# Kernel tuning notes

Hardware: AMD Instinct MI355X
Metric: run time of the kernel (lower is better)

The kernel has to match this reference:

```python
import jax, jax.numpy as jnp
import numpy as np

B, S, D, H, DH = 8, 1024, 768, 12, 64
INIT_STD = 0.02
IGNORE = -100000.0


def setup_inputs() -> dict:
    key = jax.random.key(0)
    ks = jax.random.split(key, 5)
    return {
        "normalized_resid_pre": jax.random.normal(ks[0], (B, S, D), dtype=jnp.float32),
        "W_Q": jax.random.normal(ks[1], (H, D, DH), dtype=jnp.float32) * INIT_STD,
        "b_Q": jnp.zeros((H, DH), dtype=jnp.float32),
        "W_K": jax.random.normal(ks[2], (H, D, DH), dtype=jnp.float32) * INIT_STD,
        "b_K": jnp.zeros((H, DH), dtype=jnp.float32),
        "W_V": jax.random.normal(ks[3], (H, D, DH), dtype=jnp.float32) * INIT_STD,
        "b_V": jnp.zeros((H, DH), dtype=jnp.float32),
        "W_O": jax.random.normal(ks[4], (H, DH, D), dtype=jnp.float32) * INIT_STD,
        "b_O": jnp.zeros((D,), dtype=jnp.float32),
    }


def reference(normalized_resid_pre, W_Q, b_Q, W_K, b_K, W_V, b_V, W_O, b_O):
    x = normalized_resid_pre  # [B,S,D]
    q = jnp.einsum('bsd,hde->bshe', x, W_Q) + b_Q  # [B,S,H,DH]
    k = jnp.einsum('bsd,hde->bshe', x, W_K) + b_K
    v = jnp.einsum('bsd,hde->bshe', x, W_V) + b_V
    scores = jnp.einsum('bqhe,bkhe->bhqk', q, k) / jnp.sqrt(jnp.float32(DH))
    causal = jnp.triu(jnp.ones((S, S), dtype=bool), k=1)  # True above diagonal
    scores = jnp.where(causal, jnp.float32(IGNORE), scores)
    pattern = jax.nn.softmax(scores, axis=-1)  # [B,H,S,S]
    z = jnp.einsum('bhqk,bkhe->bqhe', pattern, v)  # [B,S,H,DH]
    attn_out = jnp.einsum('bqhe,hed->bqd', z, W_O) + b_O  # [B,S,D]
    return attn_out
```

## Files before the change

kernel.cpp:

```cpp
#include <hip/hip_runtime.h>
#include <hip/hip_bf16.h>
#include <stdint.h>

#define BB 8
#define SS 1024
#define DD 768
#define HH 12
#define DHH 64
#define BS (BB*SS)
#define NQKV (3*HH*DHH)

typedef __attribute__((ext_vector_type(8))) short bf16x8;
typedef __attribute__((ext_vector_type(4))) float f32x4;
typedef __attribute__((ext_vector_type(4))) unsigned int u32x4;

typedef const __attribute__((address_space(1))) unsigned int gu32;
typedef __attribute__((address_space(3))) unsigned int lu32;

static __device__ __forceinline__ unsigned short f2bf(float f) {
    union { float f; unsigned int u; } v; v.f = f;
    unsigned int u = v.u;
    unsigned int r = (u + 0x7fffu + ((u >> 16) & 1u)) >> 16;
    return (unsigned short)r;
}

static __device__ __forceinline__ unsigned int cvt_pk_bf16(float lo, float hi) {
    unsigned int r;
    asm("v_cvt_pk_bf16_f32 %0, %1, %2" : "=v"(r) : "v"(lo), "v"(hi));
    return r;
}


__global__ void k_f32_to_bf16(const float* __restrict__ in, unsigned short* __restrict__ out, int n) {
    int i = (blockIdx.x * 256 + threadIdx.x) * 4;
    if (i + 3 < n) {
        float4 v = *reinterpret_cast<const float4*>(in + i);
        ushort4 o;
        o.x = f2bf(v.x); o.y = f2bf(v.y); o.z = f2bf(v.z); o.w = f2bf(v.w);
        *reinterpret_cast<ushort4*>(out + i) = o;
    } else {
        for (; i < n; ++i) out[i] = f2bf(in[i]);
    }
}

__global__ void k_transpose_wqkv(const float* __restrict__ wq, const float* __restrict__ wk,
                                 const float* __restrict__ wv, unsigned short* __restrict__ wt) {
    __shared__ float tl[64][65];
    int rt = blockIdx.x;
    int z = blockIdx.y;
    int mat = z / 12, h = z - mat * 12;
    const float* src = ((mat == 0) ? wq : (mat == 1) ? wk : wv) + (size_t)h * 768 * 64;
    int d0 = rt * 64;
    int t = threadIdx.x;
    int row = t >> 4, c4 = (t & 15) * 4;
    #pragma unroll
    for (int p = 0; p < 4; ++p) {
        int d = p * 16 + row;
        float4 v = *reinterpret_cast<const float4*>(&src[(size_t)(d0 + d) * 64 + c4]);
        tl[d][c4 + 0] = v.x; tl[d][c4 + 1] = v.y; tl[d][c4 + 2] = v.z; tl[d][c4 + 3] = v.w;
    }
    __syncthreads();
    unsigned short* dstb = wt + ((size_t)(mat * 768 + h * 64)) * 768;
    #pragma unroll
    for (int p = 0; p < 4; ++p) {
        int e = p * 16 + row;
        ushort4 o;
        o.x = f2bf(tl[c4 + 0][e]); o.y = f2bf(tl[c4 + 1][e]);
        o.z = f2bf(tl[c4 + 2][e]); o.w = f2bf(tl[c4 + 3][e]);
        *reinterpret_cast<ushort4*>(&dstb[(size_t)e * 768 + d0 + c4]) = o;
    }
}

__global__ void k_transpose_wo(const float* __restrict__ wo, unsigned short* __restrict__ wot) {
    __shared__ float tl[64][65];
    int r0 = blockIdx.x * 64;
    int c0 = blockIdx.y * 64;
    int t = threadIdx.x;
    int row = t >> 4, c4 = (t & 15) * 4;
    #pragma unroll
    for (int p = 0; p < 4; ++p) {
        int r = p * 16 + row;
        float4 v = *reinterpret_cast<const float4*>(&wo[(size_t)(r0 + r) * 768 + c0 + c4]);
        tl[r][c4 + 0] = v.x; tl[r][c4 + 1] = v.y; tl[r][c4 + 2] = v.z; tl[r][c4 + 3] = v.w;
    }
    __syncthreads();
    #pragma unroll
    for (int p = 0; p < 4; ++p) {
        int c = p * 16 + row;
        ushort4 o;
        o.x = f2bf(tl[c4 + 0][c]); o.y = f2bf(tl[c4 + 1][c]);
        o.z = f2bf(tl[c4 + 2][c]); o.w = f2bf(tl[c4 + 3][c]);
        *reinterpret_cast<ushort4*>(&wot[(size_t)(c0 + c) * 768 + r0 + c4]) = o;
    }
}

__global__ void k_transpose_v(const unsigned short* __restrict__ vb, unsigned short* __restrict__ vtb) {
    __shared__ unsigned short tl[64][68];
    int s0 = blockIdx.x * 64;
    int bh = blockIdx.y;
    const unsigned short* src = vb + (size_t)bh * SS * DHH;
    unsigned short* dst = vtb + (size_t)bh * DHH * SS;
    int t = threadIdx.x;
    #pragma unroll
    for (int i = 0; i < 16; ++i) {
        int idx = t + i * 256;
        int sl = idx >> 6, e = idx & 63;
        tl[sl][e] = src[(size_t)(s0 + sl) * DHH + e];
    }
    __syncthreads();
    #pragma unroll
    for (int i = 0; i < 16; ++i) {
        int idx = t + i * 256;
        int e = idx >> 6, sl = idx & 63;
        dst[(size_t)e * SS + s0 + sl] = tl[sl][e];
    }
}


__launch_bounds__(256)
__global__ void k_gemm_qkv(const unsigned short* __restrict__ xb,
                           const unsigned short* __restrict__ wt,
                           const float* __restrict__ bq, const float* __restrict__ bk,
                           const float* __restrict__ bv,
                           unsigned short* __restrict__ qb,
                           unsigned short* __restrict__ kb,
                           unsigned short* __restrict__ vb) {
    __shared__ unsigned short As[2][128 * 32];
    __shared__ unsigned short Bs[2][128 * 32];
    int r0 = blockIdx.x * 128;
    int c0 = blockIdx.y * 128;
    int t = threadIdx.x;
    int w = t >> 6, l = t & 63;
    int lr = l & 15, lg = l >> 4;
    int wr = w >> 1, wc = w & 1;
    int srow = l >> 2;
    int g8 = (((l & 3) - (l >> 3)) & 3) * 8;

    auto STAGE = [&](int buf, int k0) {
        #pragma unroll
        for (int c = 0; c < 2; ++c) {
            int seg = w * 2 + c;
            int row = seg * 16 + srow;
            __builtin_amdgcn_global_load_lds(
                (gu32*)(xb + (size_t)(r0 + row) * DD + k0 + g8),
                (lu32*)&As[buf][seg * 512], 16, 0, 0);
            __builtin_amdgcn_global_load_lds(
                (gu32*)(wt + (size_t)(c0 + row) * DD + k0 + g8),
                (lu32*)&Bs[buf][seg * 512], 16, 0, 0);
        }
    };

    f32x4 acc[4][4] = {};
    STAGE(0, 0);
    __syncthreads();
    int rdo = ((lg + (lr >> 1)) & 3) * 8;
    for (int kk = 0; kk < 24; ++kk) {
        int cur = kk & 1;
        if (kk < 23) STAGE(cur ^ 1, kk * 32 + 32);
        bf16x8 af[4], bfr[4];
        #pragma unroll
        for (int m = 0; m < 4; ++m)
            af[m] = *reinterpret_cast<const bf16x8*>(&As[cur][(wr * 64 + m * 16 + lr) * 32 + rdo]);
        #pragma unroll
        for (int n = 0; n < 4; ++n)
            bfr[n] = *reinterpret_cast<const bf16x8*>(&Bs[cur][(wc * 64 + n * 16 + lr) * 32 + rdo]);
        #pragma unroll
        for (int m = 0; m < 4; ++m)
            #pragma unroll
            for (int n = 0; n < 4; ++n)
                acc[m][n] = __builtin_amdgcn_mfma_f32_16x16x32_bf16(af[m], bfr[n], acc[m][n], 0, 0, 0);
        __syncthreads();
    }
    #pragma unroll
    for (int n = 0; n < 4; ++n) {
        int c = c0 + wc * 64 + n * 16 + lr;
        int mat = c / 768;
        int within = c - mat * 768;
        int h = within >> 6, e = within & 63;
        const float* bptr = (mat == 0) ? bq : (mat == 1) ? bk : bv;
        float bias = bptr[within];
        unsigned short* dst = (mat == 0) ? qb : (mat == 1) ? kb : vb;
        #pragma unroll
        for (int m = 0; m < 4; ++m) {
            #pragma unroll
            for (int i = 0; i < 4; ++i) {
                int r = r0 + wr * 64 + m * 16 + lg * 4 + i;
                int b_ = r >> 10, s_ = r & 1023;
                dst[(((size_t)(b_ * HH + h)) * SS + s_) * DHH + e] = f2bf(acc[m][n][i] + bias);
            }
        }
    }
}


#define PW 34

__launch_bounds__(256, 3)
__global__ void k_attn(const unsigned short* __restrict__ qb,
                       const unsigned short* __restrict__ kb,
                       const unsigned short* __restrict__ vtb,
                       unsigned short* __restrict__ zb) {
    __shared__ unsigned short Ks[2][64 * 64];
    __shared__ unsigned short Vs[2][64 * 64];
    __shared__ unsigned int Pl[4][16 * PW];
    int id = blockIdx.x;
    int p = id / 96;
    int bh = id - p * 96;
    int qi = 15 - p;
    int q0 = qi * 64;

    int t = threadIdx.x, w = t >> 6, l = t & 63;
    int lr = l & 15, lg = l >> 4;
    const unsigned short* Qh = qb + (size_t)bh * SS * DHH;
    const unsigned short* Kh = kb + (size_t)bh * SS * DHH;
    const unsigned short* Vt = vtb + (size_t)bh * DHH * SS;
    int b_ = bh / HH, h = bh - b_ * HH;
    unsigned int* Pw = &Pl[w][0];

    int sr8 = l >> 3;
    int sc = ((l & 7) ^ sr8) * 8;

    auto STAGE = [&](int buf, int kbase) {
        #pragma unroll
        for (int c = 0; c < 2; ++c) {
            int seg = w * 2 + c;
            int row = seg * 8 + sr8;
            __builtin_amdgcn_global_load_lds(
                (gu32*)(Kh + (size_t)(kbase + row) * DHH + sc),
                (lu32*)&Ks[buf][seg * 512], 16, 0, 0);
            __builtin_amdgcn_global_load_lds(
                (gu32*)(Vt + (size_t)row * SS + kbase + sc),
                (lu32*)&Vs[buf][seg * 512], 16, 0, 0);
        }
    };

    int qabs = q0 + w * 16 + lr;
    STAGE(0, 0);
    bf16x8 qf[2];
    qf[0] = *reinterpret_cast<const bf16x8*>(Qh + (size_t)qabs * DHH + lg * 8);
    qf[1] = *reinterpret_cast<const bf16x8*>(Qh + (size_t)qabs * DHH + 32 + lg * 8);

    float m_r = -3.0e38f, l_r = 0.f;
    f32x4 zacc[4] = {};
    __syncthreads();

    for (int kt = 0; kt <= qi; ++kt) {
        int k0 = kt * 64;
        int cur = kt & 1;
        if (kt < qi) STAGE(cur ^ 1, k0 + 64);

        f32x4 sac[4] = {};
        #pragma unroll
        for (int ks = 0; ks < 2; ++ks) {
            #pragma unroll
            for (int ct = 0; ct < 4; ++ct) {
                bf16x8 kfr = *reinterpret_cast<const bf16x8*>(
                    &Ks[cur][(ct * 16 + lr) * 64 + (((ks * 4 + lg) ^ (lr & 7)) * 8)]);
                sac[ct] = __builtin_amdgcn_mfma_f32_16x16x32_bf16(kfr, qf[ks], sac[ct], 0, 0, 0);
            }
        }
        bool diag = (kt == qi);
        float sv[4][4];
        float pm = -3.0e38f;
        #pragma unroll
        for (int ct = 0; ct < 4; ++ct) {
            #pragma unroll
            for (int i = 0; i < 4; ++i) {
                float x = sac[ct][i] * 0.125f;
                if (diag) {
                    int kabs = k0 + ct * 16 + lg * 4 + i;
                    if (kabs > qabs) x = -3.0e38f;
                }
                sv[ct][i] = x;
                pm = fmaxf(pm, x);
            }
        }
        pm = fmaxf(pm, __shfl_xor(pm, 16));
        pm = fmaxf(pm, __shfl_xor(pm, 32));

        if (!__all(pm <= m_r + 8.f)) {
            float mn = fmaxf(m_r, pm);
            float alpha = __expf(m_r - mn);
            m_r = mn;
            l_r *= alpha;
            float aC[4];
            #pragma unroll
            for (int i = 0; i < 4; ++i) aC[i] = __shfl(alpha, lg * 4 + i);
            #pragma unroll
            for (int et = 0; et < 4; ++et)
                #pragma unroll
                for (int i = 0; i < 4; ++i) zacc[et][i] *= aC[i];
        }

        float ps = 0.f;
        #pragma unroll
        for (int ct = 0; ct < 4; ++ct) {
            float p0 = __expf(sv[ct][0] - m_r);
            float p1 = __expf(sv[ct][1] - m_r);
            float p2 = __expf(sv[ct][2] - m_r);
            float p3 = __expf(sv[ct][3] - m_r);
            ps += (p0 + p1) + (p2 + p3);
            unsigned int pk0 = cvt_pk_bf16(p0, p1);
            unsigned int pk1 = cvt_pk_bf16(p2, p3);
            *reinterpret_cast<uint2*>(&Pw[lr * PW + ct * 8 + lg * 2]) = make_uint2(pk0, pk1);
        }
        ps += __shfl_xor(ps, 16);
        ps += __shfl_xor(ps, 32);
        l_r += ps;

        #pragma unroll
        for (int ks = 0; ks < 2; ++ks) {
            bf16x8 pa = *reinterpret_cast<const bf16x8*>(&Pw[lr * PW + ks * 16 + lg * 4]);
            #pragma unroll
            for (int et = 0; et < 4; ++et) {
                bf16x8 vf = *reinterpret_cast<const bf16x8*>(
                    &Vs[cur][(et * 16 + lr) * 64 + (((ks * 4 + lg) ^ (lr & 7)) * 8)]);
                zacc[et] = __builtin_amdgcn_mfma_f32_16x16x32_bf16(pa, vf, zacc[et], 0, 0, 0);
            }
        }
        __syncthreads();
    }

    float lC[4];
    #pragma unroll
    for (int i = 0; i < 4; ++i) lC[i] = __shfl(l_r, lg * 4 + i);
    #pragma unroll
    for (int et = 0; et < 4; ++et) {
        #pragma unroll
        for (int i = 0; i < 4; ++i) {
            int r = q0 + w * 16 + lg * 4 + i;
            float z = zacc[et][i] / lC[i];
            zb[((size_t)(b_ * SS + r)) * DD + h * DHH + et * 16 + lr] = f2bf(z);
        }
    }
}


__launch_bounds__(256)
__global__ void k_gemm_out(const unsigned short* __restrict__ zb,
                           const unsigned short* __restrict__ wot,
                           const float* __restrict__ bo,
                           float* __restrict__ out) {
    __shared__ unsigned short As[2][128 * 32];
    __shared__ unsigned short Bs[2][128 * 32];
    int r0 = blockIdx.x * 128;
    int c0 = blockIdx.y * 128;
    int t = threadIdx.x;
    int w = t >> 6, l = t & 63;
    int lr = l & 15, lg = l >> 4;
    int wr = w >> 1, wc = w & 1;
    int srow = l >> 2;
    int g8 = (((l & 3) - (l >> 3)) & 3) * 8;

    auto STAGE = [&](int buf, int k0) {
        #pragma unroll
        for (int c = 0; c < 2; ++c) {
            int seg = w * 2 + c;
            int row = seg * 16 + srow;
            __builtin_amdgcn_global_load_lds(
                (gu32*)(zb + (size_t)(r0 + row) * DD + k0 + g8),
                (lu32*)&As[buf][seg * 512], 16, 0, 0);
            __builtin_amdgcn_global_load_lds(
                (gu32*)(wot + (size_t)(c0 + row) * DD + k0 + g8),
                (lu32*)&Bs[buf][seg * 512], 16, 0, 0);
        }
    };

    f32x4 acc[4][4] = {};
    STAGE(0, 0);
    __syncthreads();
    int rdo = ((lg + (lr >> 1)) & 3) * 8;
    for (int kk = 0; kk < 24; ++kk) {
        int cur = kk & 1;
        if (kk < 23) STAGE(cur ^ 1, kk * 32 + 32);
        bf16x8 af[4], bfr[4];
        #pragma unroll
        for (int m = 0; m < 4; ++m)
            af[m] = *reinterpret_cast<const bf16x8*>(&As[cur][(wr * 64 + m * 16 + lr) * 32 + rdo]);
        #pragma unroll
        for (int n = 0; n < 4; ++n)
            bfr[n] = *reinterpret_cast<const bf16x8*>(&Bs[cur][(wc * 64 + n * 16 + lr) * 32 + rdo]);
        #pragma unroll
        for (int m = 0; m < 4; ++m)
            #pragma unroll
            for (int n = 0; n < 4; ++n)
                acc[m][n] = __builtin_amdgcn_mfma_f32_16x16x32_bf16(af[m], bfr[n], acc[m][n], 0, 0, 0);
        __syncthreads();
    }
    #pragma unroll
    for (int n = 0; n < 4; ++n) {
        int c = c0 + wc * 64 + n * 16 + lr;
        float bias = bo[c];
        #pragma unroll
        for (int m = 0; m < 4; ++m) {
            #pragma unroll
            for (int i = 0; i < 4; ++i) {
                int r = r0 + wr * 64 + m * 16 + lg * 4 + i;
                out[(size_t)r * DD + c] = acc[m][n][i] + bias;
            }
        }
    }
}


extern "C" void kernel_launch(void* const* d_in, const int* in_sizes, int n_in,
                              void* d_out, int out_size, void* d_ws, size_t ws_size,
                              hipStream_t stream) {
    const float* x  = (const float*)d_in[0];
    const float* wq = (const float*)d_in[1];
    const float* bq = (const float*)d_in[2];
    const float* wk = (const float*)d_in[3];
    const float* bk = (const float*)d_in[4];
    const float* wv = (const float*)d_in[5];
    const float* bv = (const float*)d_in[6];
    const float* wo = (const float*)d_in[7];
    const float* bo = (const float*)d_in[8];
    float* out = (float*)d_out;

    char* ws = (char*)d_ws;
    size_t off = 0;
    auto alloc = [&](size_t bytes) -> char* {
        char* p = ws + off;
        off += (bytes + 255) & ~(size_t)255;
        return p;
    };
    unsigned short* xb   = (unsigned short*)alloc((size_t)BS * DD * 2);
    unsigned short* wt   = (unsigned short*)alloc((size_t)NQKV * DD * 2);
    unsigned short* wot  = (unsigned short*)alloc((size_t)DD * DD * 2);
    unsigned short* qb   = (unsigned short*)alloc((size_t)BB * HH * SS * DHH * 2);
    unsigned short* kb   = (unsigned short*)alloc((size_t)BB * HH * SS * DHH * 2);
    unsigned short* vb   = (unsigned short*)alloc((size_t)BB * HH * SS * DHH * 2);
    unsigned short* vtb  = (unsigned short*)alloc((size_t)BB * HH * SS * DHH * 2);
    unsigned short* zb   = (unsigned short*)alloc((size_t)BS * DD * 2);
    (void)ws_size; (void)in_sizes; (void)n_in; (void)out_size;

    k_f32_to_bf16<<<dim3((BS * DD) / (256 * 4)), dim3(256), 0, stream>>>(x, xb, BS * DD);
    k_transpose_wqkv<<<dim3(12, 36), dim3(256), 0, stream>>>(wq, wk, wv, wt);
    k_transpose_wo<<<dim3(12, 12), dim3(256), 0, stream>>>(wo, wot);
    k_gemm_qkv<<<dim3(BS / 128, NQKV / 128), dim3(256), 0, stream>>>(xb, wt, bq, bk, bv, qb, kb, vb);
    k_transpose_v<<<dim3(SS / 64, BB * HH), dim3(256), 0, stream>>>(vb, vtb);
    k_attn<<<dim3(16 * 96), dim3(256), 0, stream>>>(qb, kb, vtb, zb);
    k_gemm_out<<<dim3(BS / 128, DD / 128), dim3(256), 0, stream>>>(zb, wot, bo, out);
}
```

Before: 133.4 us.

## Deepen GEMM LDS pipeline to four stages with vmcnt waits and XCD-aware tile mapping

Both projection GEMMs move from a double-buffered LDS loop with full __syncthreads to a four-buffer ring. Three tiles are kept in flight and guarded by explicit s_waitcnt vmcnt(12) plus s_barrier, so global-to-LDS loads overlap more MFMA work. The grid is also flattened to 1D and remapped so that consecutive blocks on the same XCD share row tiles, which is meant to improve L2 reuse. In exchange, LDS use per block doubles, which may lower occupancy, and correctness now depends on the hand-counted vmcnt.

Result: no change. 131.6 us (-1.3%).

```diff
diff --git a/kernel.cpp b/kernel.cpp
--- a/kernel.cpp
+++ b/kernel.cpp
@@ -29,6 +29,10 @@
     asm("v_cvt_pk_bf16_f32 %0, %1, %2" : "=v"(r) : "v"(lo), "v"(hi));
     return r;
 }
+
+#define VWBAR12() asm volatile("s_waitcnt vmcnt(12)\ns_barrier" ::: "memory")
+#define VWBAR0()  asm volatile("s_waitcnt vmcnt(0)\ns_barrier" ::: "memory")
+#define BAR()     asm volatile("s_barrier" ::: "memory")
 
 
 __global__ void k_f32_to_bf16(const float* __restrict__ in, unsigned short* __restrict__ out, int n) {
@@ -125,16 +129,23 @@
                            unsigned short* __restrict__ qb,
                            unsigned short* __restrict__ kb,
                            unsigned short* __restrict__ vb) {
-    __shared__ unsigned short As[2][128 * 32];
-    __shared__ unsigned short Bs[2][128 * 32];
-    int r0 = blockIdx.x * 128;
-    int c0 = blockIdx.y * 128;
+    __shared__ unsigned short As[4][128 * 32];
+    __shared__ unsigned short Bs[4][128 * 32];
+    int id = blockIdx.x;
+    int xcd = id & 7, j = id >> 3;
+    int bx = xcd * 8 + (j & 7);
+    int by = j >> 3;
+    int r0 = bx * 128;
+    int c0 = by * 128;
     int t = threadIdx.x;
     int w = t >> 6, l = t & 63;
     int lr = l & 15, lg = l >> 4;
     int wr = w >> 1, wc = w & 1;
     int srow = l >> 2;
     int g8 = (((l & 3) - (l >> 3)) & 3) * 8;
+    int rdo = ((lg + (lr >> 1)) & 3) * 8;
+
+    f32x4 acc[4][4] = {};
 
     auto STAGE = [&](int buf, int k0) {
         #pragma unroll
@@ -149,28 +160,37 @@
                 (lu32*)&Bs[buf][seg * 512], 16, 0, 0);
         }
     };
-
-    f32x4 acc[4][4] = {};
-    STAGE(0, 0);
-    __syncthreads();
-    int rdo = ((lg + (lr >> 1)) & 3) * 8;
-    for (int kk = 0; kk < 24; ++kk) {
-        int cur = kk & 1;
-        if (kk < 23) STAGE(cur ^ 1, kk * 32 + 32);
+    auto COMPUTE = [&](int buf) {
         bf16x8 af[4], bfr[4];
         #pragma unroll
         for (int m = 0; m < 4; ++m)
-            af[m] = *reinterpret_cast<const bf16x8*>(&As[cur][(wr * 64 + m * 16 + lr) * 32 + rdo]);
+            af[m] = *reinterpret_cast<const bf16x8*>(&As[buf][(wr * 64 + m * 16 + lr) * 32 + rdo]);
         #pragma unroll
         for (int n = 0; n < 4; ++n)
-            bfr[n] = *reinterpret_cast<const bf16x8*>(&Bs[cur][(wc * 64 + n * 16 + lr) * 32 + rdo]);
+            bfr[n] = *reinterpret_cast<const bf16x8*>(&Bs[buf][(wc * 64 + n * 16 + lr) * 32 + rdo]);
         #pragma unroll
         for (int m = 0; m < 4; ++m)
             #pragma unroll
             for (int n = 0; n < 4; ++n)
                 acc[m][n] = __builtin_amdgcn_mfma_f32_16x16x32_bf16(af[m], bfr[n], acc[m][n], 0, 0, 0);
-        __syncthreads();
-    }
+    };
+
+    STAGE(0, 0);
+    STAGE(1, 32);
+    STAGE(2, 64);
+    for (int kk4 = 0; kk4 < 5; ++kk4) {
+        int kb = kk4 * 128;
+        STAGE(3, kb + 96);  VWBAR12(); COMPUTE(0); BAR();
+        STAGE(0, kb + 128); VWBAR12(); COMPUTE(1); BAR();
+        STAGE(1, kb + 160); VWBAR12(); COMPUTE(2); BAR();
+        STAGE(2, kb + 192); VWBAR12(); COMPUTE(3); BAR();
+    }
+    STAGE(3, 736); VWBAR12(); COMPUTE(0); BAR();
+    VWBAR0();
+    COMPUTE(1);
+    COMPUTE(2);
+    COMPUTE(3);
+
     #pragma unroll
     for (int n = 0; n < 4; ++n) {
         int c = c0 + wc * 64 + n * 16 + lr;
@@ -341,16 +361,23 @@
                            const unsigned short* __restrict__ wot,
                            const float* __restrict__ bo,
                            float* __restrict__ out) {
-    __shared__ unsigned short As[2][128 * 32];
-    __shared__ unsigned short Bs[2][128 * 32];
-    int r0 = blockIdx.x * 128;
-    int c0 = blockIdx.y * 128;
+    __shared__ unsigned short As[4][128 * 32];
+    __shared__ unsigned short Bs[4][128 * 32];
+    int id = blockIdx.x;
+    int xcd = id & 7, j = id >> 3;
+    int bx = xcd * 8 + (j & 7);
+    int by = j >> 3;
+    int r0 = bx * 128;
+    int c0 = by * 128;
     int t = threadIdx.x;
     int w = t >> 6, l = t & 63;
     int lr = l & 15, lg = l >> 4;
     int wr = w >> 1, wc = w & 1;
     int srow = l >> 2;
     int g8 = (((l & 3) - (l >> 3)) & 3) * 8;
+    int rdo = ((lg + (lr >> 1)) & 3) * 8;
+
+    f32x4 acc[4][4] = {};
 
     auto STAGE = [&](int buf, int k0) {
         #pragma unroll
@@ -365,28 +392,37 @@
                 (lu32*)&Bs[buf][seg * 512], 16, 0, 0);
         }
     };
-
-    f32x4 acc[4][4] = {};
-    STAGE(0, 0);
-    __syncthreads();
-    int rdo = ((lg + (lr >> 1)) & 3) * 8;
-    for (int kk = 0; kk < 24; ++kk) {
-        int cur = kk & 1;
-        if (kk < 23) STAGE(cur ^ 1, kk * 32 + 32);
+    auto COMPUTE = [&](int buf) {
         bf16x8 af[4], bfr[4];
         #pragma unroll
         for (int m = 0; m < 4; ++m)
-            af[m] = *reinterpret_cast<const bf16x8*>(&As[cur][(wr * 64 + m * 16 + lr) * 32 + rdo]);
+            af[m] = *reinterpret_cast<const bf16x8*>(&As[buf][(wr * 64 + m * 16 + lr) * 32 + rdo]);
         #pragma unroll
         for (int n = 0; n < 4; ++n)
-            bfr[n] = *reinterpret_cast<const bf16x8*>(&Bs[cur][(wc * 64 + n * 16 + lr) * 32 + rdo]);
+            bfr[n] = *reinterpret_cast<const bf16x8*>(&Bs[buf][(wc * 64 + n * 16 + lr) * 32 + rdo]);
         #pragma unroll
         for (int m = 0; m < 4; ++m)
             #pragma unroll
             for (int n = 0; n < 4; ++n)
                 acc[m][n] = __builtin_amdgcn_mfma_f32_16x16x32_bf16(af[m], bfr[n], acc[m][n], 0, 0, 0);
-        __syncthreads();
-    }
+    };
+
+    STAGE(0, 0);
+    STAGE(1, 32);
+    STAGE(2, 64);
+    for (int kk4 = 0; kk4 < 5; ++kk4) {
+        int kb = kk4 * 128;
+        STAGE(3, kb + 96);  VWBAR12(); COMPUTE(0); BAR();
+        STAGE(0, kb + 128); VWBAR12(); COMPUTE(1); BAR();
+        STAGE(1, kb + 160); VWBAR12(); COMPUTE(2); BAR();
+        STAGE(2, kb + 192); VWBAR12(); COMPUTE(3); BAR();
+    }
+    STAGE(3, 736); VWBAR12(); COMPUTE(0); BAR();
+    VWBAR0();
+    COMPUTE(1);
+    COMPUTE(2);
+    COMPUTE(3);
+
     #pragma unroll
     for (int n = 0; n < 4; ++n) {
         int c = c0 + wc * 64 + n * 16 + lr;
@@ -437,8 +473,8 @@
     k_f32_to_bf16<<<dim3((BS * DD) / (256 * 4)), dim3(256), 0, stream>>>(x, xb, BS * DD);
     k_transpose_wqkv<<<dim3(12, 36), dim3(256), 0, stream>>>(wq, wk, wv, wt);
     k_transpose_wo<<<dim3(12, 12), dim3(256), 0, stream>>>(wo, wot);
-    k_gemm_qkv<<<dim3(BS / 128, NQKV / 128), dim3(256), 0, stream>>>(xb, wt, bq, bk, bv, qb, kb, vb);
+    k_gemm_qkv<<<dim3(1152), dim3(256), 0, stream>>>(xb, wt, bq, bk, bv, qb, kb, vb);
     k_transpose_v<<<dim3(SS / 64, BB * HH), dim3(256), 0, stream>>>(vb, vtb);
     k_attn<<<dim3(16 * 96), dim3(256), 0, stream>>>(qb, kb, vtb, zb);
-    k_gemm_out<<<dim3(BS / 128, DD / 128), dim3(256), 0, stream>>>(zb, wot, bo, out);
-}
+    k_gemm_out<<<dim3(384), dim3(256), 0, stream>>>(zb, wot, bo, out);
+}
```
